# Optimization experiments

Hardware: AMD Instinct MI355X
Metric: run time of the kernel (lower is better)

## Reference

```python
import jax, jax.numpy as jnp
import numpy as np
from jax import lax

DN = ('NCHW', 'OIHW', 'NCHW')

def _conv(x, w, b, stride, pad):
    y = lax.conv_general_dilated(x, w, (stride, stride), ((pad, pad), (pad, pad)),
                                 dimension_numbers=DN)
    return y + b[None, :, None, None]

def _convT(x, w, b):
    # torch ConvTranspose2d(k=4, s=2, p=1); w: (C_in, C_out, 4, 4)
    wt = jnp.transpose(jnp.flip(w, (2, 3)), (1, 0, 2, 3))  # (C_out, C_in, 4, 4)
    y = lax.conv_general_dilated(x, wt, (1, 1), ((2, 2), (2, 2)),
                                 lhs_dilation=(2, 2), dimension_numbers=DN)
    return y + b[None, :, None, None]

def setup_inputs() -> dict:
    key = jax.random.key(0)
    ks = jax.random.split(key, 20)
    s = 0.05
    inp = {
        'x':   jax.random.normal(ks[0], (8, 1, 256, 256), jnp.float32),
        'ew1': jax.random.normal(ks[1], (64, 1, 3, 3), jnp.float32) * s,
        'eb1': jnp.zeros((64,), jnp.float32),
        'ew2': jax.random.normal(ks[2], (128, 64, 3, 3), jnp.float32) * s,
        'eb2': jnp.zeros((128,), jnp.float32),
        'ew3': jax.random.normal(ks[3], (256, 128, 3, 3), jnp.float32) * s,
        'eb3': jnp.zeros((256,), jnp.float32),
        'ew4': jax.random.normal(ks[4], (256, 256, 1, 1), jnp.float32) * s,
        'eb4': jnp.zeros((256,), jnp.float32),
        # torch init: uniform(-1/K, 1/K) with K=1024
        'codebook': jax.random.uniform(ks[5], (1024, 256), jnp.float32,
                                       minval=-1.0 / 1024, maxval=1.0 / 1024),
        'dw1': jax.random.normal(ks[6], (256, 256, 1, 1), jnp.float32) * s,
        'db1': jnp.zeros((256,), jnp.float32),
        'dw2': jax.random.normal(ks[7], (256, 128, 4, 4), jnp.float32) * s,
        'db2': jnp.zeros((128,), jnp.float32),
        'dw3': jax.random.normal(ks[8], (128, 64, 4, 4), jnp.float32) * s,
        'db3': jnp.zeros((64,), jnp.float32),
        'dw4': jax.random.normal(ks[9], (1, 64, 3, 3), jnp.float32) * s,
        'db4': jnp.zeros((1,), jnp.float32),
        'scale_idx': 2,
    }
    return inp

def reference(x, ew1, eb1, ew2, eb2, ew3, eb3, ew4, eb4, codebook,
              dw1, db1, dw2, db2, dw3, db3, dw4, db4, scale_idx):
    # ---- encoder (scale_idx=2: 1->64->128->256->embedding_dim) ----
    h = jax.nn.relu(_conv(x, ew1, eb1, 1, 1))        # [B,64,256,256]
    h = jax.nn.relu(_conv(h, ew2, eb2, 2, 1))        # [B,128,128,128]
    h = jax.nn.relu(_conv(h, ew3, eb3, 2, 1))        # [B,256,64,64]
    z = _conv(h, ew4, eb4, 1, 0)                     # [B,D,64,64]
    # ---- vector quantization ----
    B, D, H, W = z.shape
    flat = jnp.transpose(z, (0, 2, 3, 1)).reshape(-1, D)        # [N,D]
    dist = (jnp.sum(flat * flat, axis=1, keepdims=True)
            + jnp.sum(codebook * codebook, axis=1)
            - 2.0 * flat @ codebook.T)                          # [N,K]
    idx = jnp.argmin(dist, axis=1)                              # [N]
    quantized = codebook[idx].reshape(B, H, W, D)               # gather == onehot@codebook
    z_q = jnp.transpose(quantized, (0, 3, 1, 2))                # [B,D,H,W]
    indices = idx.reshape(B, H, W)
    # ---- decoder ----
    d = jax.nn.relu(_conv(z_q, dw1, db1, 1, 0))      # [B,256,64,64]
    d = jax.nn.relu(_convT(d, dw2, db2))             # [B,128,128,128]
    d = jax.nn.relu(_convT(d, dw3, db3))             # [B,64,256,256]
    recon = jax.nn.sigmoid(_conv(d, dw4, db4, 1, 1)) # [B,1,256,256]
    return recon, z_q, indices
```

## Files before the change

### kernel.cpp

```cpp
#include <hip/hip_runtime.h>
#include <hip/hip_bf16.h>
#include <math.h>


#define NB 8

typedef short v8s __attribute__((ext_vector_type(8)));
typedef float v4f __attribute__((ext_vector_type(4)));

__device__ __forceinline__ float sumsq128(const float* __restrict__ p, int stride) {
  float r[8];
#pragma unroll
  for (int j = 0; j < 8; ++j) {
    float v = p[(size_t)j * stride];
    r[j] = __fmul_rn(v, v);
  }
  for (int i = 8; i < 128; i += 8) {
#pragma unroll
    for (int j = 0; j < 8; ++j) {
      float v = p[(size_t)(i + j) * stride];
      r[j] = __fadd_rn(r[j], __fmul_rn(v, v));
    }
  }
  return __fadd_rn(__fadd_rn(__fadd_rn(r[0], r[1]), __fadd_rn(r[2], r[3])),
                   __fadd_rn(__fadd_rn(r[4], r[5]), __fadd_rn(r[6], r[7])));
}
__device__ __forceinline__ float sumsq256(const float* __restrict__ p, int stride) {
  return __fadd_rn(sumsq128(p, stride), sumsq128(p + (size_t)128 * stride, stride));
}

__global__ __launch_bounds__(256) void k_conv12(const float* __restrict__ x,
                                                const float* __restrict__ ew1,
                                                const float* __restrict__ eb1,
                                                const float* __restrict__ ew2,
                                                const float* __restrict__ bias2,
                                                float* __restrict__ out) {
  const int IH = 256;
  const int OH = 128;
  const int TILES_X = OH / 16;
  int n = blockIdx.z;
  int cg = blockIdx.y;
  int tile = blockIdx.x;
  int OY0 = (tile / TILES_X) * 16, OX0 = (tile % TILES_X) * 16;
  int ty = threadIdx.x >> 4, tx = threadIdx.x & 15;
  int oy = OY0 + ty, ox = OX0 + tx;

  const float* xin = x + (size_t)n * IH * IH;
  float xv[5][5];
#pragma unroll
  for (int a = 0; a < 5; ++a)
#pragma unroll
    for (int b = 0; b < 5; ++b) {
      int iy = 2 * oy - 2 + a, ix = 2 * ox - 2 + b;
      xv[a][b] = (iy >= 0 && iy < IH && ix >= 0 && ix < IH) ? xin[iy * IH + ix] : 0.f;
    }

  unsigned hmask = 0;
#pragma unroll
  for (int dy = 0; dy < 3; ++dy)
#pragma unroll
    for (int dx = 0; dx < 3; ++dx) {
      int hy = 2 * oy - 1 + dy, hx = 2 * ox - 1 + dx;
      if (hy >= 0 && hy < IH && hx >= 0 && hx < IH) hmask |= 1u << (dy * 3 + dx);
    }

  float acc[32];
#pragma unroll
  for (int c = 0; c < 32; ++c) acc[c] = 0.f;

  for (int ci = 0; ci < 64; ++ci) {
    const float* w1 = ew1 + ci * 9;
    float b1 = eb1[ci];
    float v[9];
#pragma unroll
    for (int dy = 0; dy < 3; ++dy)
#pragma unroll
      for (int dx = 0; dx < 3; ++dx) {
        int k = dy * 3 + dx;
        if (hmask & (1u << k)) {
          float h = b1;
#pragma unroll
          for (int ey = 0; ey < 3; ++ey)
#pragma unroll
            for (int ex = 0; ex < 3; ++ex) h += xv[dy + ey][dx + ex] * w1[ey * 3 + ex];
          v[k] = fmaxf(h, 0.f);
        } else {
          v[k] = 0.f;
        }
      }
    const float* wp = ew2 + ((size_t)(cg * 32) * 64 + ci) * 9;
#pragma unroll
    for (int c = 0; c < 32; ++c) {
#pragma unroll
      for (int k = 0; k < 9; ++k) acc[c] += v[k] * wp[(size_t)c * 64 * 9 + k];
    }
  }
  float* ob = out + (((size_t)n * 128 + cg * 32) * OH + oy) * OH + ox;
#pragma unroll
  for (int c = 0; c < 32; ++c) {
    float r = acc[c] + bias2[cg * 32 + c];
    ob[(size_t)c * OH * OH] = fmaxf(r, 0.f);
  }
}

template <int CI, int IH>
__global__ __launch_bounds__(256) void k_conv3s2(const float* __restrict__ in,
                                                 const float* __restrict__ w,
                                                 const float* __restrict__ bias,
                                                 float* __restrict__ out, int CO) {
  const int OH = IH / 2;
  const int TILES_X = OH / 16;
  const int RS = 40;
  int n = blockIdx.z;
  int cg = blockIdx.y;
  int tile = blockIdx.x;
  int OY0 = (tile / TILES_X) * 16, OX0 = (tile % TILES_X) * 16;
  int ty = threadIdx.x >> 4, tx = threadIdx.x & 15;
  __shared__ float sm[2][33 * RS];
  float acc[32];
#pragma unroll
  for (int c = 0; c < 32; ++c) acc[c] = 0.f;
  int iy0 = 2 * OY0 - 1, ix0 = 2 * OX0 - 1;
  const float* inb = in + (size_t)n * CI * IH * IH;

  for (int t = threadIdx.x; t < 2 * 33 * RS; t += 256) (&sm[0][0])[t] = 0.f;

  int goff[5], loff[5];
  unsigned vmask = 0;
#pragma unroll
  for (int i = 0; i < 5; ++i) {
    int t = threadIdx.x + 256 * i;
    if (t < 33 * 33) {
      int r = t / 33, c = t - r * 33;
      int iy = iy0 + r, ix = ix0 + c;
      if (iy >= 0 && iy < IH && ix >= 0 && ix < IH) {
        vmask |= 1u << i;
        goff[i] = iy * IH + ix;
        loff[i] = r * RS + (c >> 1) + (c & 1) * 17;
      }
    }
  }
  __syncthreads();

  auto stage = [&](int buf, int ci) {
    const float* ip = inb + (size_t)ci * IH * IH;
    float* dst = sm[buf];
#pragma unroll
    for (int i = 0; i < 5; ++i)
      if (vmask & (1u << i)) dst[loff[i]] = ip[goff[i]];
  };
  stage(0, 0);
  for (int ci = 0; ci < CI; ++ci) {
    int buf = ci & 1;
    __syncthreads();
    if (ci + 1 < CI) stage(buf ^ 1, ci + 1);
    float v[9];
#pragma unroll
    for (int dy = 0; dy < 3; ++dy)
#pragma unroll
      for (int dx = 0; dx < 3; ++dx)
        v[dy * 3 + dx] = sm[buf][(2 * ty + dy) * RS + (dx & 1) * 17 + tx + (dx >> 1)];
    const float* wp = w + ((size_t)(cg * 32) * CI + ci) * 9;
#pragma unroll
    for (int c = 0; c < 32; ++c) {
#pragma unroll
      for (int k = 0; k < 9; ++k) acc[c] += v[k] * wp[(size_t)c * CI * 9 + k];
    }
  }
  int oy = OY0 + ty, ox = OX0 + tx;
  float* ob = out + (((size_t)n * CO + cg * 32) * OH + oy) * OH + ox;
#pragma unroll
  for (int c = 0; c < 32; ++c) {
    float r = acc[c] + bias[cg * 32 + c];
    ob[(size_t)c * OH * OH] = fmaxf(r, 0.f);
  }
}

__global__ __launch_bounds__(256) void k_conv1x1(const float* __restrict__ in,
                                                 const float* __restrict__ w,
                                                 const float* __restrict__ bias,
                                                 float* __restrict__ out, int CI, int CO,
                                                 int HW) {
  int n = blockIdx.z;
  int cg = blockIdx.y;
  int px = blockIdx.x * 256 + threadIdx.x;
  __shared__ float sm[16][256];
  const float* inb = in + (size_t)n * CI * HW;
  float acc[8];
#pragma unroll
  for (int c = 0; c < 8; ++c) acc[c] = 0.f;
  for (int c0 = 0; c0 < CI; c0 += 16) {
#pragma unroll
    for (int i = 0; i < 16; ++i) sm[i][threadIdx.x] = inb[(size_t)(c0 + i) * HW + px];
    __syncthreads();
    const float* wb = w + (size_t)(cg * 8) * CI + c0;
#pragma unroll
    for (int i = 0; i < 16; ++i) {
      float r = sm[i][threadIdx.x];
#pragma unroll
      for (int c = 0; c < 8; ++c) acc[c] += r * wb[(size_t)c * CI + i];
    }
    __syncthreads();
  }
#pragma unroll
  for (int c = 0; c < 8; ++c) {
    float r = acc[c] + bias[cg * 8 + c];
    out[((size_t)n * CO + cg * 8 + c) * HW + px] = r;
  }
}

__global__ __launch_bounds__(256) void k_cnorm(const float* __restrict__ cb,
                                               float* __restrict__ cn) {
  int j = blockIdx.x * 256 + threadIdx.x;
  if (j < 1024) cn[j] = sumsq256(cb + (size_t)j * 256, 1);
}

__global__ __launch_bounds__(256) void k_xnorm(const float* __restrict__ z,
                                               float* __restrict__ xn) {
  int t = blockIdx.x * 256 + threadIdx.x;
  int n = t >> 12, yx = t & 4095;
  xn[t] = sumsq256(z + (size_t)n * 256 * 4096 + yx, 4096);
}

__global__ __launch_bounds__(256) void k_vq(const float* __restrict__ z,
                                            const float* __restrict__ cb,
                                            const float* __restrict__ cn,
                                            const float* __restrict__ xn,
                                            int* __restrict__ idx,
                                            float* __restrict__ idxf) {
  __shared__ __align__(16) float zt[64][68];
  __shared__ float ct[64][65];
  __shared__ float cnt[64];
  __shared__ float xnt[64];
  __shared__ float rbest[64][17];
  __shared__ int ribest[64][17];
  int tid = threadIdx.x;
  int pq = tid & 15;
  int cq = tid >> 4;
  int p0 = blockIdx.x * 64;
  int n = p0 >> 12;
  int yx0 = p0 & 4095;
  const float* zb = z + (size_t)n * 256 * 4096 + yx0;
  if (tid < 64) xnt[tid] = xn[p0 + tid];
  float best[4] = {3.0e38f, 3.0e38f, 3.0e38f, 3.0e38f};
  int bidx[4] = {0, 0, 0, 0};
  for (int c0 = 0; c0 < 1024; c0 += 64) {
    float acc[4][4];
#pragma unroll
    for (int a = 0; a < 4; ++a)
#pragma unroll
      for (int b = 0; b < 4; ++b) acc[a][b] = 0.f;
    for (int k0 = 0; k0 < 256; k0 += 64) {
      __syncthreads();
      for (int t = tid; t < 4096; t += 256) {
        int r = t >> 6, c = t & 63;
        zt[r][c] = zb[(size_t)(k0 + r) * 4096 + c];
      }
      for (int t = tid; t < 4096; t += 256) {
        int c = t >> 6, r = t & 63;
        ct[c][r] = cb[(size_t)(c0 + c) * 256 + k0 + r];
      }
      if (k0 == 0 && tid < 64) cnt[tid] = cn[c0 + tid];
      __syncthreads();
#pragma unroll 8
      for (int k = 0; k < 64; ++k) {
        const float4 zz = *reinterpret_cast<const float4*>(&zt[k][pq * 4]);
#pragma unroll
        for (int j = 0; j < 4; ++j) {
          float cv = ct[cq * 4 + j][k];
          acc[0][j] += zz.x * cv;
          acc[1][j] += zz.y * cv;
          acc[2][j] += zz.z * cv;
          acc[3][j] += zz.w * cv;
        }
      }
    }
#pragma unroll
    for (int pi = 0; pi < 4; ++pi) {
      float xnp = xnt[pq * 4 + pi];
#pragma unroll
      for (int j = 0; j < 4; ++j) {
        float A = __fadd_rn(xnp, cnt[cq * 4 + j]);
        float d = __fsub_rn(A, __fmul_rn(2.0f, acc[pi][j]));
        if (d < best[pi]) {
          best[pi] = d;
          bidx[pi] = c0 + cq * 4 + j;
        }
      }
    }
  }
  __syncthreads();
#pragma unroll
  for (int pi = 0; pi < 4; ++pi) {
    rbest[pq * 4 + pi][cq] = best[pi];
    ribest[pq * 4 + pi][cq] = bidx[pi];
  }
  __syncthreads();
  if (tid < 64) {
    float bv = rbest[tid][0];
    int bj = ribest[tid][0];
    for (int g = 1; g < 16; ++g) {
      float v = rbest[tid][g];
      int j2 = ribest[tid][g];
      if (v < bv || (v == bv && j2 < bj)) { bv = v; bj = j2; }
    }
    idx[p0 + tid] = bj;
    idxf[p0 + tid] = (float)bj;
  }
}

__global__ __launch_bounds__(256) void k_gather(const int* __restrict__ idx,
                                                const float* __restrict__ cb,
                                                float* __restrict__ zq,
                                                __hip_bfloat16* __restrict__ zqbf) {
  size_t g = (size_t)blockIdx.x * 256 + threadIdx.x;
  int yx4 = (int)(g & 1023);
  int d = (int)((g >> 10) & 255);
  int n = (int)(g >> 18);
  int pbase = (n << 12) | (yx4 << 2);
  int4 ii = *reinterpret_cast<const int4*>(&idx[pbase]);
  float4 v;
  v.x = cb[(size_t)ii.x * 256 + d];
  v.y = cb[(size_t)ii.y * 256 + d];
  v.z = cb[(size_t)ii.z * 256 + d];
  v.w = cb[(size_t)ii.w * 256 + d];
  size_t o = (((size_t)n * 256 + d) << 12) | (size_t)(yx4 << 2);
  *reinterpret_cast<float4*>(&zq[o]) = v;
  ushort4 bv;
  __hip_bfloat16 b0 = __float2bfloat16(v.x), b1 = __float2bfloat16(v.y);
  __hip_bfloat16 b2 = __float2bfloat16(v.z), b3 = __float2bfloat16(v.w);
  bv.x = *reinterpret_cast<ushort*>(&b0);
  bv.y = *reinterpret_cast<ushort*>(&b1);
  bv.z = *reinterpret_cast<ushort*>(&b2);
  bv.w = *reinterpret_cast<ushort*>(&b3);
  *reinterpret_cast<ushort4*>(&zqbf[o]) = bv;
}

__global__ __launch_bounds__(256) void k_wconv(const float* __restrict__ w,
                                               __hip_bfloat16* __restrict__ wA,
                                               int CI, int CO) {
  int t = blockIdx.x * 256 + threadIdx.x;
  int total = 4 * CO * CI * 4;
  if (t >= total) return;
  int tap = t & 3;
  int q = t >> 2;
  int ci = q % CI;
  int pc = q / CI;
  int co = pc % CO;
  int par = pc / CO;
  int a = tap >> 1, b = tap & 1, ry = par >> 1, rx = par & 1;
  float v = w[((size_t)ci * CO + co) * 16 + (3 - ry - 2 * a) * 4 + (3 - rx - 2 * b)];
  wA[t] = __float2bfloat16(v);
}

__global__ __launch_bounds__(256) void k_wconv1(const float* __restrict__ w,
                                                __hip_bfloat16* __restrict__ wb) {
  int t = blockIdx.x * 256 + threadIdx.x;
  if (t < 65536) wb[t] = __float2bfloat16(w[t]);
}

__global__ __launch_bounds__(256) void k_d1mfma(const __hip_bfloat16* __restrict__ in,
                                                const __hip_bfloat16* __restrict__ wb,
                                                const float* __restrict__ bias,
                                                __hip_bfloat16* __restrict__ out) {
  int n = blockIdx.z;
  int co0 = blockIdx.y * 64;
  int px0 = blockIdx.x * 64;
  int tid = threadIdx.x;
  int w = tid >> 6, lane = tid & 63, fr = lane & 15, kg = lane >> 4;

  __shared__ __align__(16) ushort Wt[64][40];
  __shared__ __align__(16) ushort Zt[64][40];

  v4f acc[4];
#pragma unroll
  for (int q = 0; q < 4; ++q) acc[q] = (v4f){0.f, 0.f, 0.f, 0.f};

  const ushort* inb = (const ushort*)in + (size_t)n * 256 * 4096;
  const ushort* wab = (const ushort*)wb;

  for (int k0 = 0; k0 < 256; k0 += 32) {
    __syncthreads();
    {
      int co = tid & 63, kgg = tid >> 6;
      const uint4 v = *(const uint4*)(wab + (size_t)(co0 + co) * 256 + k0 + kgg * 8);
      *(uint4*)&Wt[co][kgg * 8] = v;
    }
    {
      int ci = tid >> 3, pxg = tid & 7;
      const ushort* src = inb + (size_t)(k0 + ci) * 4096 + px0 + pxg * 8;
      uint4 v = *(const uint4*)src;
      const ushort* vs = (const ushort*)&v;
#pragma unroll
      for (int j = 0; j < 8; ++j) Zt[pxg * 8 + j][ci] = vs[j];
    }
    __syncthreads();
    v8s af = *(const v8s*)&Wt[w * 16 + fr][kg * 8];
#pragma unroll
    for (int q = 0; q < 4; ++q) {
      v8s b = *(const v8s*)&Zt[q * 16 + fr][kg * 8];
      acc[q] = __builtin_amdgcn_mfma_f32_16x16x32_bf16(af, b, acc[q], 0, 0, 0);
    }
  }
  __hip_bfloat16* ob = out + (size_t)n * 256 * 4096;
#pragma unroll
  for (int q = 0; q < 4; ++q) {
    int px = px0 + q * 16 + fr;
#pragma unroll
    for (int r = 0; r < 4; ++r) {
      int co = co0 + w * 16 + kg * 4 + r;
      float val = fmaxf(acc[q][r] + bias[co], 0.f);
      ob[(size_t)co * 4096 + px] = __float2bfloat16(val);
    }
  }
}

template <int CI, int IH, int CO>
__global__ __launch_bounds__(256) void k_convTmfma(const __hip_bfloat16* __restrict__ in,
                                                   const __hip_bfloat16* __restrict__ wA,
                                                   const float* __restrict__ bias,
                                                   __hip_bfloat16* __restrict__ out) {
  const int OH = 2 * IH;
  const int NT = IH / 32;
  int n = blockIdx.z;
  int co0 = blockIdx.y * 64;
  int m = blockIdx.x / NT;
  int n0x = (blockIdx.x % NT) * 32;
  int tid = threadIdx.x;
  int w = tid >> 6, lane = tid & 63, fr = lane & 15, kg = lane >> 4;

  __shared__ __align__(16) ushort Wt[4][64][40];
  __shared__ __align__(16) ushort Bt[4][32][40];
  __shared__ ushort patch[8][3][36];

  v4f acc[4][2];
#pragma unroll
  for (int p = 0; p < 4; ++p)
#pragma unroll
    for (int h = 0; h < 2; ++h) acc[p][h] = (v4f){0.f, 0.f, 0.f, 0.f};

  const ushort* inb = (const ushort*)in + (size_t)n * CI * IH * IH;
  const ushort* wab = (const ushort*)wA;

  for (int t = tid; t < 8 * 3 * 36; t += 256) (&patch[0][0][0])[t] = 0;

  int pgoff[4], ploff[4];
  unsigned pmask = 0;
#pragma unroll
  for (int i = 0; i < 4; ++i) {
    int t = tid + 256 * i;
    if (t < 816) {
      int ci = t / 102;
      int rem = t - ci * 102;
      int r = rem / 34;
      int c = rem - r * 34;
      int iy = m - 1 + r, ix = n0x - 1 + c;
      if (iy >= 0 && iy < IH && ix >= 0 && ix < IH) {
        pmask |= 1u << i;
        pgoff[i] = (ci * IH + iy) * IH + ix;
        ploff[i] = (ci * 3 + r) * 36 + c;
      }
    }
  }

  for (int ci0 = 0; ci0 < CI; ci0 += 8) {
    __syncthreads();
    {
      const ushort* ip = inb + (size_t)ci0 * IH * IH;
      ushort* pb = &patch[0][0][0];
#pragma unroll
      for (int i = 0; i < 4; ++i)
        if (pmask & (1u << i)) pb[ploff[i]] = ip[pgoff[i]];
    }
#pragma unroll
    for (int i = 0; i < 4; ++i) {
      int u = tid + 256 * i;
      int kgg = u & 3, co = (u >> 2) & 63, par = u >> 8;
      const uint4 v =
          *(const uint4*)(wab + (((size_t)par * CO + co0 + co) * CI + ci0) * 4 + kgg * 8);
      *(uint4*)&Wt[par][co][kgg * 8] = v;
    }
    __syncthreads();
    {
      int pr = tid >> 1;
      int px0 = (tid & 1) * 16;
      int par = pr >> 5, k = pr & 31;
      int ci = k >> 2, a = (k >> 1) & 1, b = k & 1, ry = par >> 1, rx = par & 1;
      const ushort* src = &patch[ci][ry + a][px0 + rx + b];
      ushort* dst = &Bt[par][px0][k];
#pragma unroll
      for (int p = 0; p < 16; ++p) dst[p * 40] = src[p];
    }
    __syncthreads();
#pragma unroll
    for (int par = 0; par < 4; ++par) {
      v8s af = *(const v8s*)&Wt[par][w * 16 + fr][kg * 8];
      v8s b0 = *(const v8s*)&Bt[par][fr][kg * 8];
      v8s b1 = *(const v8s*)&Bt[par][16 + fr][kg * 8];
      acc[par][0] = __builtin_amdgcn_mfma_f32_16x16x32_bf16(af, b0, acc[par][0], 0, 0, 0);
      acc[par][1] = __builtin_amdgcn_mfma_f32_16x16x32_bf16(af, b1, acc[par][1], 0, 0, 0);
    }
  }
  __hip_bfloat16* ob = out + (size_t)n * CO * OH * OH;
#pragma unroll
  for (int par = 0; par < 4; ++par) {
    int ry = par >> 1, rx = par & 1;
    int oy = 2 * m + ry;
#pragma unroll
    for (int h = 0; h < 2; ++h) {
      int ox = 2 * (n0x + h * 16 + fr) + rx;
#pragma unroll
      for (int r = 0; r < 4; ++r) {
        int co = co0 + w * 16 + kg * 4 + r;
        float val = acc[par][h][r] + bias[co];
        val = fmaxf(val, 0.f);
        ob[((size_t)co * OH + oy) * OH + ox] = __float2bfloat16(val);
      }
    }
  }
}

__global__ __launch_bounds__(256) void k_conv_out(const __hip_bfloat16* __restrict__ in,
                                                  const float* __restrict__ w,
                                                  const float* __restrict__ bias,
                                                  float* __restrict__ out) {
  int n = blockIdx.z;
  int tile = blockIdx.x;
  int TY0 = (tile / 16) * 16, TX0 = (tile % 16) * 16;
  int ty = threadIdx.x >> 4, tx = threadIdx.x & 15;
  __shared__ float sm[2][18 * 18];
  float acc = bias[0];
  const __hip_bfloat16* inb = in + (size_t)n * 64 * 65536;
  int goff[2], loff[2];
  unsigned vmask = 0;
#pragma unroll
  for (int i = 0; i < 2; ++i) {
    int t = threadIdx.x + 256 * i;
    if (t < 324) {
      int r = t / 18, c = t - r * 18;
      int iy = TY0 - 1 + r, ix = TX0 - 1 + c;
      if (iy >= 0 && iy < 256 && ix >= 0 && ix < 256) {
        vmask |= 1u << i;
        goff[i] = iy * 256 + ix;
        loff[i] = t;
      }
    }
  }
  for (int t = threadIdx.x; t < 2 * 324; t += 256) (&sm[0][0])[t] = 0.f;
  __syncthreads();
  auto stage = [&](int buf, int ci) {
    const __hip_bfloat16* ip = inb + (size_t)ci * 65536;
    float* dst = sm[buf];
#pragma unroll
    for (int i = 0; i < 2; ++i)
      if (vmask & (1u << i)) dst[loff[i]] = __bfloat162float(ip[goff[i]]);
  };
  stage(0, 0);
  for (int ci = 0; ci < 64; ++ci) {
    int buf = ci & 1;
    __syncthreads();
    if (ci + 1 < 64) stage(buf ^ 1, ci + 1);
    const float* wp = w + ci * 9;
#pragma unroll
    for (int dy = 0; dy < 3; ++dy)
#pragma unroll
      for (int dx = 0; dx < 3; ++dx) acc += sm[buf][(ty + dy) * 18 + tx + dx] * wp[dy * 3 + dx];
  }
  out[(size_t)n * 65536 + (TY0 + ty) * 256 + TX0 + tx] = 1.f / (1.f + expf(-acc));
}

extern "C" void kernel_launch(void* const* d_in, const int* in_sizes, int n_in,
                              void* d_out, int out_size, void* d_ws, size_t ws_size,
                              hipStream_t stream) {
  const float* x = (const float*)d_in[0];
  const float* ew1 = (const float*)d_in[1];
  const float* eb1 = (const float*)d_in[2];
  const float* ew2 = (const float*)d_in[3];
  const float* eb2 = (const float*)d_in[4];
  const float* ew3 = (const float*)d_in[5];
  const float* eb3 = (const float*)d_in[6];
  const float* ew4 = (const float*)d_in[7];
  const float* eb4 = (const float*)d_in[8];
  const float* cb = (const float*)d_in[9];
  const float* dw1 = (const float*)d_in[10];
  const float* db1 = (const float*)d_in[11];
  const float* dw2 = (const float*)d_in[12];
  const float* db2 = (const float*)d_in[13];
  const float* dw3 = (const float*)d_in[14];
  const float* db3 = (const float*)d_in[15];
  const float* dw4 = (const float*)d_in[16];
  const float* db4 = (const float*)d_in[17];

  float* ws = (float*)d_ws;
  float* A = ws;
  float* Bb = ws + 33554432;
  float* Cc = ws + 50331648;
  float* cn = A + 16777216;
  float* xn = A + 16778240;
  int* idx = (int*)(A + 16811008);
  __hip_bfloat16* zqbf = (__hip_bfloat16*)(A + 20971520);
  __hip_bfloat16* wbfA2 = (__hip_bfloat16*)(A + 25165824);
  __hip_bfloat16* wbfA3 = (__hip_bfloat16*)(A + 25427968);
  __hip_bfloat16* wbf1 = (__hip_bfloat16*)(A + 25493504);
  __hip_bfloat16* d1bf = (__hip_bfloat16*)Cc;
  __hip_bfloat16* d2bf = (__hip_bfloat16*)Bb;
  __hip_bfloat16* d3bf = (__hip_bfloat16*)A;

  float* recon = (float*)d_out;
  float* zq = recon + 524288;
  float* idxf = zq + 8388608;

  k_conv12<<<dim3(64, 4, NB), 256, 0, stream>>>(x, ew1, eb1, ew2, eb2, Bb);
  k_conv3s2<128, 128><<<dim3(16, 8, NB), 256, 0, stream>>>(Bb, ew3, eb3, Cc, 256);
  k_conv1x1<<<dim3(16, 32, NB), 256, 0, stream>>>(Cc, ew4, eb4, A, 256, 256, 4096);
  k_wconv<<<2048, 256, 0, stream>>>(dw2, wbfA2, 256, 128);
  k_wconv<<<512, 256, 0, stream>>>(dw3, wbfA3, 128, 64);
  k_wconv1<<<256, 256, 0, stream>>>(dw1, wbf1);
  k_cnorm<<<4, 256, 0, stream>>>(cb, cn);
  k_xnorm<<<128, 256, 0, stream>>>(A, xn);
  k_vq<<<512, 256, 0, stream>>>(A, cb, cn, xn, idx, idxf);
  k_gather<<<8192, 256, 0, stream>>>(idx, cb, zq, zqbf);
  k_d1mfma<<<dim3(64, 4, NB), 256, 0, stream>>>(zqbf, wbf1, db1, d1bf);
  k_convTmfma<256, 64, 128><<<dim3(128, 2, NB), 256, 0, stream>>>(d1bf, wbfA2, db2, d2bf);
  k_convTmfma<128, 128, 64><<<dim3(512, 1, NB), 256, 0, stream>>>(d2bf, wbfA3, db3, d3bf);
  k_conv_out<<<dim3(256, 1, NB), 256, 0, stream>>>(d3bf, dw4, db4, recon);
}
```

Measured before the change: 1.839 ms.

## Compute 2x2 output patch per thread in fused conv1+conv2 to reuse conv1 values

Each thread now produces a 2x2 block of conv2 outputs for 16 channels instead of one output for 32 channels. It computes a shared 5x5 window of conv1 activations from a 7x7 input patch. This cuts redundant conv1 recomputation and input loads per output, and lets the stores be written as float2. The trade-off is higher register use (xv, h and 64 accumulators), which could lower occupancy or cause spills.

```diff
diff --git a/kernel.cpp b/kernel.cpp
--- a/kernel.cpp
+++ b/kernel.cpp
@@ -37,69 +37,84 @@
                                                 float* __restrict__ out) {
   const int IH = 256;
   const int OH = 128;
-  const int TILES_X = OH / 16;
   int n = blockIdx.z;
   int cg = blockIdx.y;
   int tile = blockIdx.x;
-  int OY0 = (tile / TILES_X) * 16, OX0 = (tile % TILES_X) * 16;
+  int TY0 = (tile >> 2) * 32, TX0 = (tile & 3) * 32;
   int ty = threadIdx.x >> 4, tx = threadIdx.x & 15;
-  int oy = OY0 + ty, ox = OX0 + tx;
+  int oy0 = TY0 + 2 * ty, ox0 = TX0 + 2 * tx;
 
   const float* xin = x + (size_t)n * IH * IH;
-  float xv[5][5];
+  float xv[7][7];
+#pragma unroll
+  for (int a = 0; a < 7; ++a)
+#pragma unroll
+    for (int b = 0; b < 7; ++b) {
+      int iy = 2 * oy0 - 2 + a, ix = 2 * ox0 - 2 + b;
+      xv[a][b] = (iy >= 0 && iy < IH && ix >= 0 && ix < IH) ? xin[iy * IH + ix] : 0.f;
+    }
+
+  unsigned hmask = 0;
 #pragma unroll
   for (int a = 0; a < 5; ++a)
 #pragma unroll
     for (int b = 0; b < 5; ++b) {
-      int iy = 2 * oy - 2 + a, ix = 2 * ox - 2 + b;
-      xv[a][b] = (iy >= 0 && iy < IH && ix >= 0 && ix < IH) ? xin[iy * IH + ix] : 0.f;
-    }
-
-  unsigned hmask = 0;
-#pragma unroll
-  for (int dy = 0; dy < 3; ++dy)
-#pragma unroll
-    for (int dx = 0; dx < 3; ++dx) {
-      int hy = 2 * oy - 1 + dy, hx = 2 * ox - 1 + dx;
-      if (hy >= 0 && hy < IH && hx >= 0 && hx < IH) hmask |= 1u << (dy * 3 + dx);
-    }
-
-  float acc[32];
-#pragma unroll
-  for (int c = 0; c < 32; ++c) acc[c] = 0.f;
+      int hy = 2 * oy0 - 1 + a, hx = 2 * ox0 - 1 + b;
+      if (hy >= 0 && hy < IH && hx >= 0 && hx < IH) hmask |= 1u << (a * 5 + b);
+    }
+
+  float acc[4][16];
+#pragma unroll
+  for (int p = 0; p < 4; ++p)
+#pragma unroll
+    for (int c = 0; c < 16; ++c) acc[p][c] = 0.f;
 
   for (int ci = 0; ci < 64; ++ci) {
     const float* w1 = ew1 + ci * 9;
     float b1 = eb1[ci];
-    float v[9];
-#pragma unroll
-    for (int dy = 0; dy < 3; ++dy)
-#pragma unroll
-      for (int dx = 0; dx < 3; ++dx) {
-        int k = dy * 3 + dx;
-        if (hmask & (1u << k)) {
-          float h = b1;
+    float h[5][5];
+#pragma unroll
+    for (int a = 0; a < 5; ++a)
+#pragma unroll
+      for (int b = 0; b < 5; ++b) {
+        if (hmask & (1u << (a * 5 + b))) {
+          float hh = b1;
 #pragma unroll
           for (int ey = 0; ey < 3; ++ey)
 #pragma unroll
-            for (int ex = 0; ex < 3; ++ex) h += xv[dy + ey][dx + ex] * w1[ey * 3 + ex];
-          v[k] = fmaxf(h, 0.f);
+            for (int ex = 0; ex < 3; ++ex) hh += xv[a + ey][b + ex] * w1[ey * 3 + ex];
+          h[a][b] = fmaxf(hh, 0.f);
         } else {
-          v[k] = 0.f;
+          h[a][b] = 0.f;
         }
       }
-    const float* wp = ew2 + ((size_t)(cg * 32) * 64 + ci) * 9;
-#pragma unroll
-    for (int c = 0; c < 32; ++c) {
-#pragma unroll
-      for (int k = 0; k < 9; ++k) acc[c] += v[k] * wp[(size_t)c * 64 * 9 + k];
-    }
-  }
-  float* ob = out + (((size_t)n * 128 + cg * 32) * OH + oy) * OH + ox;
-#pragma unroll
-  for (int c = 0; c < 32; ++c) {
-    float r = acc[c] + bias2[cg * 32 + c];
-    ob[(size_t)c * OH * OH] = fmaxf(r, 0.f);
+    const float* wp = ew2 + ((size_t)(cg * 16) * 64 + ci) * 9;
+#pragma unroll
+    for (int c = 0; c < 16; ++c) {
+      const float* wc = wp + (size_t)c * 64 * 9;
+#pragma unroll
+      for (int py = 0; py < 2; ++py)
+#pragma unroll
+        for (int qx = 0; qx < 2; ++qx) {
+#pragma unroll
+          for (int dy = 0; dy < 3; ++dy)
+#pragma unroll
+            for (int dx = 0; dx < 3; ++dx)
+              acc[py * 2 + qx][c] += h[2 * py + dy][2 * qx + dx] * wc[dy * 3 + dx];
+        }
+    }
+  }
+#pragma unroll
+  for (int c = 0; c < 16; ++c) {
+    float bb = bias2[cg * 16 + c];
+    float* ob = out + (((size_t)n * 128 + cg * 16 + c) * OH + oy0) * OH + ox0;
+#pragma unroll
+    for (int py = 0; py < 2; ++py) {
+      float2 v2;
+      v2.x = fmaxf(acc[py * 2 + 0][c] + bb, 0.f);
+      v2.y = fmaxf(acc[py * 2 + 1][c] + bb, 0.f);
+      *reinterpret_cast<float2*>(ob + (size_t)py * OH) = v2;
+    }
   }
 }
 
@@ -610,7 +625,7 @@
   float* zq = recon + 524288;
   float* idxf = zq + 8388608;
 
-  k_conv12<<<dim3(64, 4, NB), 256, 0, stream>>>(x, ew1, eb1, ew2, eb2, Bb);
+  k_conv12<<<dim3(16, 8, NB), 256, 0, stream>>>(x, ew1, eb1, ew2, eb2, Bb);
   k_conv3s2<128, 128><<<dim3(16, 8, NB), 256, 0, stream>>>(Bb, ew3, eb3, Cc, 256);
   k_conv1x1<<<dim3(16, 32, NB), 256, 0, stream>>>(Cc, ew4, eb4, A, 256, 256, 4096);
   k_wconv<<<2048, 256, 0, stream>>>(dw2, wbfA2, 256, 128);
```

Result: no change. 1.871 ms (+1.7%).
